# Kernel optimization log

Measured on AMD Instinct MI355X. Metric: run time of the kernel, lower is better.

## Reference

```python
import jax, jax.numpy as jnp
import numpy as np

N_NODES = 50000
N_EDGES = 800000


def setup_inputs() -> dict:
    key = jax.random.key(0)
    ks = jax.random.split(key, 10)
    x = jax.random.normal(ks[0], (N_NODES, 256), dtype=jnp.float32)
    edge_index = jax.random.randint(ks[1], (2, N_EDGES), 0, N_NODES, dtype=jnp.int64)
    edge_attr = jax.random.uniform(ks[2], (N_EDGES,), dtype=jnp.float32)
    def glorot(k, fan_in, fan_out):
        s = jnp.sqrt(6.0 / (fan_in + fan_out))
        return jax.random.uniform(k, (fan_in, fan_out), minval=-s, maxval=s, dtype=jnp.float32)
    W1 = glorot(ks[3], 256, 512); b1 = jnp.zeros((512,), jnp.float32)
    W2 = glorot(ks[4], 512, 256); b2 = jnp.zeros((256,), jnp.float32)
    W3 = glorot(ks[5], 256, 128); b3 = jnp.zeros((128,), jnp.float32)
    return {"x": x, "edge_index": edge_index, "edge_attr": edge_attr,
            "W1": W1, "b1": b1, "W2": W2, "b2": b2, "W3": W3, "b3": b3}


def _gcn_norm(edge_index, edge_attr, num_nodes):
    # PyG GCNConv default: add self-loops (weight 1), symmetric normalization.
    loops = jnp.arange(num_nodes, dtype=edge_index.dtype)
    src = jnp.concatenate([edge_index[0], loops])
    dst = jnp.concatenate([edge_index[1], loops])
    w = jnp.concatenate([edge_attr, jnp.ones((num_nodes,), edge_attr.dtype)])
    deg = jax.ops.segment_sum(w, dst, num_segments=num_nodes)
    dinv = jnp.where(deg > 0, jax.lax.rsqrt(deg), 0.0)
    norm = dinv[src] * w * dinv[dst]  # [E+N]
    return src, dst, norm


def _gcn_conv(h, W, b, src, dst, norm, num_nodes):
    h = h @ W                                   # [N, Dout] linear transform
    msg = h[src] * norm[:, None]                # gather + per-edge scale
    out = jax.ops.segment_sum(msg, dst, num_segments=num_nodes)  # scatter-add
    return out + b


def reference(x, edge_index, edge_attr, W1, b1, W2, b2, W3, b3):
    src, dst, norm = _gcn_norm(edge_index, edge_attr, N_NODES)
    h = jax.nn.relu(_gcn_conv(x, W1, b1, src, dst, norm, N_NODES))
    # dropout is identity in eval mode (reference runs with training=False)
    h = jax.nn.relu(_gcn_conv(h, W2, b2, src, dst, norm, N_NODES))
    h = _gcn_conv(h, W3, b3, src, dst, norm, N_NODES)
    return h.reshape(-1, h.shape[1])
```

## Files before the change

kernel.cpp:

```cpp
#include <hip/hip_runtime.h>
#include <cstdint>
#include <cstddef>

typedef unsigned short u16;
typedef unsigned int u32;

#define NN 50000
#define NE 800000

typedef __attribute__((ext_vector_type(8))) short bf16x8;
typedef __attribute__((ext_vector_type(4))) float f32x4;

__device__ __forceinline__ u16 f2bf(float f) {
  union { float f; u32 i; } v; v.f = f;
  return (u16)((v.i + 0x7FFFu + ((v.i >> 16) & 1u)) >> 16);
}
__device__ __forceinline__ void bf2x2(u32 w, float& a, float& b) {
  union { u32 i; float f; } lo, hi;
  lo.i = w << 16; hi.i = w & 0xFFFF0000u;
  a = lo.f; b = hi.f;
}
__device__ __forceinline__ void unpack8(const uint4& q, float* f) {
  bf2x2(q.x, f[0], f[1]); bf2x2(q.y, f[2], f[3]);
  bf2x2(q.z, f[4], f[5]); bf2x2(q.w, f[6], f[7]);
}

#define HIST_B 3125
#define XGROUPS (NN * 256 / 4)

__global__ void k_hist_cast(const int* __restrict__ dst,
                            int* __restrict__ cnt, int* __restrict__ slot,
                            const float* __restrict__ x, const float* __restrict__ W1,
                            const float* __restrict__ W2, const float* __restrict__ W3,
                            u16* __restrict__ xb, u16* __restrict__ Wt1,
                            u16* __restrict__ Wt2, u16* __restrict__ Wt3) {
  int b = blockIdx.x;
  if (b < HIST_B) {
    int e = b * 256 + threadIdx.x;
    if (e < NE) slot[e] = atomicAdd(&cnt[dst[e]], 1);
  } else {
    int i = (b - HIST_B) * 256 + threadIdx.x;
    if (i < XGROUPS) {
      float4 f = ((const float4*)x)[i];
      uint2 u;
      u.x = (u32)f2bf(f.x) | ((u32)f2bf(f.y) << 16);
      u.y = (u32)f2bf(f.z) | ((u32)f2bf(f.w) << 16);
      ((uint2*)xb)[i] = u;
    } else {
      int j = i - XGROUPS;
      if (j < 131072) {
        int k = j >> 9, n = j & 511;
        Wt1[n * 256 + k] = f2bf(W1[j]);
      } else if (j < 262144) {
        int j2 = j - 131072;
        int k = j2 >> 8, n = j2 & 255;
        Wt2[n * 512 + k] = f2bf(W2[j2]);
      } else if (j < 294912) {
        int j2 = j - 262144;
        int k = j2 >> 7, n = j2 & 127;
        Wt3[n * 256 + k] = f2bf(W3[j2]);
      }
    }
  }
}

__global__ void k_scan_part(const int* __restrict__ cnt, int* __restrict__ bsum, int n) {
  __shared__ int s[256];
  int i = blockIdx.x * 256 + threadIdx.x;
  s[threadIdx.x] = (i < n) ? cnt[i] : 0;
  __syncthreads();
  for (int o = 128; o > 0; o >>= 1) {
    if (threadIdx.x < o) s[threadIdx.x] += s[threadIdx.x + o];
    __syncthreads();
  }
  if (threadIdx.x == 0) bsum[blockIdx.x] = s[0];
}
__global__ void k_scan_fin(const int* __restrict__ cnt, const int* __restrict__ bsum,
                           int* __restrict__ rowptr, int n) {
  __shared__ int s[256];
  __shared__ int pre[256];
  int t = threadIdx.x;
  int i = blockIdx.x * 256 + t;
  pre[t] = (t < blockIdx.x) ? bsum[t] : 0;
  s[t] = (i < n) ? cnt[i] : 0;
  __syncthreads();
  for (int o = 128; o > 0; o >>= 1) {
    if (t < o) pre[t] += pre[t + o];
    __syncthreads();
  }
  if (t == 0) {
    int run = pre[0];
    for (int j = 0; j < 256; j++) { int v = s[j]; s[j] = run; run += v; }
  }
  __syncthreads();
  if (i < n) rowptr[i] = s[t];
}
__global__ void k_fill(const int* __restrict__ src, const int* __restrict__ dst,
                       const float* __restrict__ w, const int* __restrict__ rowptr,
                       const int* __restrict__ slot, uint2* __restrict__ edges, int E) {
  int e = blockIdx.x * 256 + threadIdx.x;
  if (e < E) {
    int d = dst[e];
    uint2 ev;
    ev.x = (u32)src[e];
    ev.y = __float_as_uint(w[e]);
    edges[rowptr[d] + slot[e]] = ev;
  }
}

__global__ __launch_bounds__(256) void k_sortrow(
    uint2* __restrict__ edges, const int* __restrict__ rowptr,
    const int* __restrict__ cnt, float* __restrict__ dinv, int n) {
  int wave = threadIdx.x >> 6, lane = threadIdx.x & 63;
  int row = blockIdx.x * 4 + wave;
  if (row >= n) return;
  int p = rowptr[row], c = cnt[row];
  if (c <= 64) {
    u32 kc = 0xFFFFFFFFu, kw = 0xFFFFFFFFu;
    if (lane < c) { uint2 e = edges[p + lane]; kc = e.x; kw = e.y; }
#pragma unroll
    for (int k = 2; k <= 64; k <<= 1) {
#pragma unroll
      for (int j = k >> 1; j > 0; j >>= 1) {
        u32 oc = __shfl_xor(kc, j, 64);
        u32 ow = __shfl_xor(kw, j, 64);
        bool up = ((lane & k) == 0);
        bool lower = ((lane & j) == 0);
        bool gt = (kc > oc) || (kc == oc && kw > ow);
        bool lt = (kc < oc) || (kc == oc && kw < ow);
        bool swap = up ? (lower ? gt : lt) : (lower ? lt : gt);
        if (swap) { kc = oc; kw = ow; }
      }
    }
    float s = (lane < c) ? __uint_as_float(kw) : 0.f;
#pragma unroll
    for (int off = 1; off < 64; off <<= 1) s += __shfl_xor(s, off, 64);
    if (lane < c) { uint2 e; e.x = kc; e.y = kw; edges[p + lane] = e; }
    if (lane == 0) dinv[row] = rsqrtf(1.0f + s);
  } else {
    if (lane == 0) {
      for (int i = 1; i < c; i++) {
        uint2 key = edges[p + i];
        int j2 = i - 1;
        while (j2 >= 0) {
          uint2 a = edges[p + j2];
          bool gt = (a.x > key.x) || (a.x == key.x && a.y > key.y);
          if (!gt) break;
          edges[p + j2 + 1] = a; j2--;
        }
        edges[p + j2 + 1] = key;
      }
      float s = 0.f;
      for (int i = 0; i < c; i++) s += __uint_as_float(edges[p + i].y);
      dinv[row] = rsqrtf(1.0f + s);
    }
  }
}

__global__ __launch_bounds__(256) void k_val(
    uint2* __restrict__ edges, const int* __restrict__ rowptr,
    const int* __restrict__ cnt, const float* __restrict__ dinv, int n) {
  int wave = threadIdx.x >> 6, lane = threadIdx.x & 63;
  int row = blockIdx.x * 4 + wave;
  if (row >= n) return;
  int p = rowptr[row], c = cnt[row];
  float dr = dinv[row];
  for (int l = lane; l < c; l += 64) {
    uint2 e = edges[p + l];
    float w = __uint_as_float(e.y);
    e.y = __float_as_uint(dinv[(int)e.x] * w * dr);
    edges[p + l] = e;
  }
}

template <int D, int OUTF32, int RELU, int HASB, int U>
__global__ __launch_bounds__(128) void k_agg(
    const u16* __restrict__ H, const int* __restrict__ rowptr,
    const int* __restrict__ cnt, const uint2* __restrict__ edges,
    const float* __restrict__ dinv,
    const float* __restrict__ bias, void* __restrict__ outv) {
  constexpr int RL = D / 8;
  constexpr int EPW = 64 / RL;
  int wave = threadIdx.x >> 6, lane = threadIdx.x & 63;
  int node = blockIdx.x * 2 + wave;
  if (node >= NN) return;
  const int sub = lane / RL;
  const int rl = lane & (RL - 1);
  const int base = rl * 8;
  float acc[8] = {};
  if (sub == 0) {
    float dv = dinv[node];
    float sw = dv * dv;
    uint4 q = *(const uint4*)(H + (size_t)node * D + base);
    float f[8]; unpack8(q, f);
#pragma unroll
    for (int j = 0; j < 8; j++) acc[j] = sw * f[j];
  }
  const int p = rowptr[node], c = cnt[node];
  for (int e0 = 0; e0 < c; e0 += EPW * U) {
    uint4 q[U];
    float v[U];
#pragma unroll
    for (int u = 0; u < U; u++) {
      int id = e0 + sub + u * EPW;
      bool ok = id < c;
      uint2 ev = edges[p + (ok ? id : 0)];
      v[u] = ok ? __uint_as_float(ev.y) : 0.f;
      int cs = ok ? (int)ev.x : node;
      q[u] = *(const uint4*)(H + (size_t)cs * D + base);
    }
#pragma unroll
    for (int u = 0; u < U; u++) {
      float f[8]; unpack8(q[u], f);
#pragma unroll
      for (int j = 0; j < 8; j++) acc[j] += v[u] * f[j];
    }
  }
#pragma unroll
  for (int j = 0; j < 8; j++) {
#pragma unroll
    for (int off = RL; off < 64; off <<= 1)
      acc[j] += __shfl_xor(acc[j], off, 64);
  }
  if (sub == 0) {
#pragma unroll
    for (int j = 0; j < 8; j++) {
      float v2 = acc[j];
      if (HASB) v2 += bias[base + j];
      if (RELU) v2 = fmaxf(v2, 0.f);
      acc[j] = v2;
    }
    if (OUTF32) {
      float* o = (float*)outv + (size_t)node * D + base;
      float4 f0 = {acc[0], acc[1], acc[2], acc[3]};
      float4 f1 = {acc[4], acc[5], acc[6], acc[7]};
      *(float4*)o = f0;
      *(float4*)(o + 4) = f1;
    } else {
      u16* o = (u16*)outv + (size_t)node * D + base;
      uint4 u;
      u.x = (u32)f2bf(acc[0]) | ((u32)f2bf(acc[1]) << 16);
      u.y = (u32)f2bf(acc[2]) | ((u32)f2bf(acc[3]) << 16);
      u.z = (u32)f2bf(acc[4]) | ((u32)f2bf(acc[5]) << 16);
      u.w = (u32)f2bf(acc[6]) | ((u32)f2bf(acc[7]) << 16);
      *(uint4*)o = u;
    }
  }
}

template <int RELU, int HASB, int NYB>
__global__ __launch_bounds__(512) void k_gemm(
    const u16* __restrict__ A, const u16* __restrict__ Bt,
    const float* __restrict__ bias, u16* __restrict__ C, int M, int Nd, int K) {
  __shared__ u16 As[256 * 64];
  __shared__ u16 Bs[128 * 64];
  const int tid = threadIdx.x;
  const int wave = tid >> 6, lane = tid & 63;
  const int nwg = gridDim.x;
  const int orig = blockIdx.x;
  const int xcd = orig & 7;
  const int q = nwg >> 3, r = nwg & 7;
  const int wgid = (xcd < r ? xcd * (q + 1) : r * (q + 1) + (xcd - r) * q) + (orig >> 3);
  const int m0 = (wgid / NYB) * 256, n0 = (wgid % NYB) * 128;
  const int wr = wave >> 1, wc = wave & 1;
  f32x4 acc[4][4] = {};

  for (int k0 = 0; k0 < K; k0 += 64) {
#pragma unroll
    for (int i = 0; i < 4; i++) {
      int rr = i * 64 + wave * 8 + (lane >> 3);
      int rg = m0 + rr; rg = rg < M ? rg : M - 1;
      const u16* ga = A + (size_t)rg * K + k0 + (lane & 7) * 8;
      __builtin_amdgcn_global_load_lds(
          (const __attribute__((address_space(1))) void*)ga,
          (__attribute__((address_space(3))) void*)&As[(i * 64 + wave * 8) * 64], 16, 0, 0);
    }
#pragma unroll
    for (int i = 0; i < 2; i++) {
      int rr = i * 64 + wave * 8 + (lane >> 3);
      int ng = n0 + rr;
      const u16* gb = Bt + (size_t)ng * K + k0 + (lane & 7) * 8;
      __builtin_amdgcn_global_load_lds(
          (const __attribute__((address_space(1))) void*)gb,
          (__attribute__((address_space(3))) void*)&Bs[(i * 64 + wave * 8) * 64], 16, 0, 0);
    }
    __syncthreads();
#pragma unroll
    for (int kk = 0; kk < 2; kk++) {
      bf16x8 af[4], bfr[4];
#pragma unroll
      for (int mi = 0; mi < 4; mi++)
        af[mi] = *(const bf16x8*)&As[(wr * 64 + mi * 16 + (lane & 15)) * 64 + kk * 32 + (lane >> 4) * 8];
#pragma unroll
      for (int ni = 0; ni < 4; ni++)
        bfr[ni] = *(const bf16x8*)&Bs[(wc * 64 + ni * 16 + (lane & 15)) * 64 + kk * 32 + (lane >> 4) * 8];
#pragma unroll
      for (int mi = 0; mi < 4; mi++)
#pragma unroll
        for (int ni = 0; ni < 4; ni++)
          acc[mi][ni] = __builtin_amdgcn_mfma_f32_16x16x32_bf16(af[mi], bfr[ni], acc[mi][ni], 0, 0, 0);
    }
    __syncthreads();
  }
  const int nb = n0 + wc * 64 + (lane & 15);
  float bv[4];
#pragma unroll
  for (int ni = 0; ni < 4; ni++) bv[ni] = HASB ? bias[nb + ni * 16] : 0.f;
#pragma unroll
  for (int mi = 0; mi < 4; mi++) {
#pragma unroll
    for (int rr = 0; rr < 4; rr++) {
      int row = m0 + wr * 64 + mi * 16 + (lane >> 4) * 4 + rr;
      if (row < M) {
#pragma unroll
        for (int ni = 0; ni < 4; ni++) {
          float v = acc[mi][ni][rr] + bv[ni];
          if (RELU) v = fmaxf(v, 0.f);
          C[(size_t)row * Nd + nb + ni * 16] = f2bf(v);
        }
      }
    }
  }
}

extern "C" void kernel_launch(void* const* d_in, const int* in_sizes, int n_in,
                              void* d_out, int out_size, void* d_ws, size_t ws_size,
                              hipStream_t stream) {
  const float* x  = (const float*)d_in[0];
  const int*   ei = (const int*)d_in[1];
  const float* ea = (const float*)d_in[2];
  const float* W1 = (const float*)d_in[3];
  const float* b1 = (const float*)d_in[4];
  const float* W2 = (const float*)d_in[5];
  const float* b2 = (const float*)d_in[6];
  const float* W3 = (const float*)d_in[7];
  const float* b3 = (const float*)d_in[8];
  const int* e_src = ei;
  const int* e_dst = ei + NE;

  size_t off = 0;
  auto carve = [&](size_t bytes) -> void* {
    void* r = (char*)d_ws + off;
    off += (bytes + 255) & ~(size_t)255;
    return r;
  };
  int*   counts = (int*)carve(NN * 4);
  float* dinv   = (float*)carve(NN * 4);
  int*   rowptr = (int*)carve(NN * 4);
  int*   bsum   = (int*)carve(256 * 4);
  int*   slot   = (int*)carve((size_t)NE * 4);
  uint2* edges  = (uint2*)carve((size_t)NE * 8);
  u16*   Wt1    = (u16*)carve(512 * 256 * 2);
  u16*   Wt2    = (u16*)carve(256 * 512 * 2);
  u16*   Wt3    = (u16*)carve(128 * 256 * 2);
  u16*   R0     = (u16*)carve((size_t)NN * 256 * 2);
  u16*   R1     = (u16*)carve((size_t)NN * 256 * 2);
  u16*   R2     = (u16*)carve((size_t)NN * 512 * 2);

  const int NB_N = (NN + 255) / 256;
  const int NB_E = (NE + 255) / 256;
  const int ROW_B = (NN + 3) / 4;
  const int AGG_B = (NN + 1) / 2;

  hipMemsetAsync(counts, 0, (size_t)NN * 4, stream);

  k_hist_cast<<<HIST_B + (XGROUPS + 294912 + 255) / 256, 256, 0, stream>>>(
      e_dst, counts, slot, x, W1, W2, W3, R0, Wt1, Wt2, Wt3);
  k_scan_part<<<NB_N, 256, 0, stream>>>(counts, bsum, NN);
  k_scan_fin<<<NB_N, 256, 0, stream>>>(counts, bsum, rowptr, NN);
  k_fill<<<NB_E, 256, 0, stream>>>(e_src, e_dst, ea, rowptr, slot, edges, NE);
  k_sortrow<<<ROW_B, 256, 0, stream>>>(edges, rowptr, counts, dinv, NN);
  k_val<<<ROW_B, 256, 0, stream>>>(edges, rowptr, counts, dinv, NN);

  k_agg<256, 0, 0, 0, 4><<<AGG_B, 128, 0, stream>>>(R0, rowptr, counts, edges, dinv, nullptr, R1);
  k_gemm<1, 1, 4><<<196 * 4, 512, 0, stream>>>(R1, Wt1, b1, R2, NN, 512, 256);
  k_gemm<0, 0, 2><<<196 * 2, 512, 0, stream>>>(R2, Wt2, nullptr, R0, NN, 256, 512);
  k_agg<256, 0, 1, 1, 4><<<AGG_B, 128, 0, stream>>>(R0, rowptr, counts, edges, dinv, b2, R1);
  k_gemm<0, 0, 1><<<196 * 1, 512, 0, stream>>>(R1, Wt3, nullptr, R0, NN, 128, 256);
  k_agg<128, 1, 0, 1, 4><<<AGG_B, 128, 0, stream>>>(R0, rowptr, counts, edges, dinv, b3, d_out);
}
```

Baseline: 345.8 us.

## Fuse edge-norm computation into first aggregation and interleave histogram with cast blocks

Removes the separate k_val kernel. The first aggregation pass now computes each edge's normalized weight from dinv, uses it, and writes it back into the edge list so the later passes can read it precomputed. The histogram/atomic blocks are also interleaved among the cast blocks, one in every 18 blocks, with each thread handling 4 edges, so that atomic traffic overlaps with streaming casts. The cost is an extra dinv gather plus an edge write inside the first aggregation, and extra index arithmetic in the block mapping.

```diff
diff --git a/kernel.cpp b/kernel.cpp
--- a/kernel.cpp
+++ b/kernel.cpp
@@ -25,8 +25,9 @@
   bf2x2(q.z, f[4], f[5]); bf2x2(q.w, f[6], f[7]);
 }
 
-#define HIST_B 3125
 #define XGROUPS (NN * 256 / 4)
+#define NA_B 782
+#define T_B 14455
 
 __global__ void k_hist_cast(const int* __restrict__ dst,
                             int* __restrict__ cnt, int* __restrict__ slot,
@@ -35,11 +36,27 @@
                             u16* __restrict__ xb, u16* __restrict__ Wt1,
                             u16* __restrict__ Wt2, u16* __restrict__ Wt3) {
   int b = blockIdx.x;
-  if (b < HIST_B) {
-    int e = b * 256 + threadIdx.x;
-    if (e < NE) slot[e] = atomicAdd(&cnt[dst[e]], 1);
+  int q = b / 18, r = b - q * 18;
+  if (r == 17) {
+    if (q >= NA_B) return;
+    int ebase = q * 1024 + threadIdx.x;
+    int ds[4]; bool ok[4];
+#pragma unroll
+    for (int u = 0; u < 4; u++) {
+      int e = ebase + u * 256;
+      ok[u] = e < NE;
+      ds[u] = ok[u] ? dst[e] : 0;
+    }
+    int sl[4];
+#pragma unroll
+    for (int u = 0; u < 4; u++)
+      if (ok[u]) sl[u] = atomicAdd(&cnt[ds[u]], 1);
+#pragma unroll
+    for (int u = 0; u < 4; u++)
+      if (ok[u]) slot[ebase + u * 256] = sl[u];
   } else {
-    int i = (b - HIST_B) * 256 + threadIdx.x;
+    int ci = b - q;
+    int i = ci * 256 + threadIdx.x;
     if (i < XGROUPS) {
       float4 f = ((const float4*)x)[i];
       uint2 u;
@@ -157,26 +174,10 @@
   }
 }
 
-__global__ __launch_bounds__(256) void k_val(
-    uint2* __restrict__ edges, const int* __restrict__ rowptr,
-    const int* __restrict__ cnt, const float* __restrict__ dinv, int n) {
-  int wave = threadIdx.x >> 6, lane = threadIdx.x & 63;
-  int row = blockIdx.x * 4 + wave;
-  if (row >= n) return;
-  int p = rowptr[row], c = cnt[row];
-  float dr = dinv[row];
-  for (int l = lane; l < c; l += 64) {
-    uint2 e = edges[p + l];
-    float w = __uint_as_float(e.y);
-    e.y = __float_as_uint(dinv[(int)e.x] * w * dr);
-    edges[p + l] = e;
-  }
-}
-
-template <int D, int OUTF32, int RELU, int HASB, int U>
+template <int D, int OUTF32, int RELU, int HASB, int U, int NORMIFY>
 __global__ __launch_bounds__(128) void k_agg(
     const u16* __restrict__ H, const int* __restrict__ rowptr,
-    const int* __restrict__ cnt, const uint2* __restrict__ edges,
+    const int* __restrict__ cnt, uint2* __restrict__ edges,
     const float* __restrict__ dinv,
     const float* __restrict__ bias, void* __restrict__ outv) {
   constexpr int RL = D / 8;
@@ -187,10 +188,10 @@
   const int sub = lane / RL;
   const int rl = lane & (RL - 1);
   const int base = rl * 8;
+  const float dvr = dinv[node];
   float acc[8] = {};
   if (sub == 0) {
-    float dv = dinv[node];
-    float sw = dv * dv;
+    float sw = dvr * dvr;
     uint4 q = *(const uint4*)(H + (size_t)node * D + base);
     float f[8]; unpack8(q, f);
 #pragma unroll
@@ -205,7 +206,16 @@
       int id = e0 + sub + u * EPW;
       bool ok = id < c;
       uint2 ev = edges[p + (ok ? id : 0)];
-      v[u] = ok ? __uint_as_float(ev.y) : 0.f;
+      float vv;
+      if (NORMIFY) {
+        int cs0 = (int)ev.x;
+        float wv = __uint_as_float(ev.y);
+        vv = dinv[cs0] * wv * dvr;
+        if (ok && rl == 0) edges[p + id].y = __float_as_uint(vv);
+      } else {
+        vv = __uint_as_float(ev.y);
+      }
+      v[u] = ok ? vv : 0.f;
       int cs = ok ? (int)ev.x : node;
       q[u] = *(const uint4*)(H + (size_t)cs * D + base);
     }
@@ -364,18 +374,17 @@
 
   hipMemsetAsync(counts, 0, (size_t)NN * 4, stream);
 
-  k_hist_cast<<<HIST_B + (XGROUPS + 294912 + 255) / 256, 256, 0, stream>>>(
+  k_hist_cast<<<T_B, 256, 0, stream>>>(
       e_dst, counts, slot, x, W1, W2, W3, R0, Wt1, Wt2, Wt3);
   k_scan_part<<<NB_N, 256, 0, stream>>>(counts, bsum, NN);
   k_scan_fin<<<NB_N, 256, 0, stream>>>(counts, bsum, rowptr, NN);
   k_fill<<<NB_E, 256, 0, stream>>>(e_src, e_dst, ea, rowptr, slot, edges, NE);
   k_sortrow<<<ROW_B, 256, 0, stream>>>(edges, rowptr, counts, dinv, NN);
-  k_val<<<ROW_B, 256, 0, stream>>>(edges, rowptr, counts, dinv, NN);
-
-  k_agg<256, 0, 0, 0, 4><<<AGG_B, 128, 0, stream>>>(R0, rowptr, counts, edges, dinv, nullptr, R1);
+
+  k_agg<256, 0, 0, 0, 4, 1><<<AGG_B, 128, 0, stream>>>(R0, rowptr, counts, edges, dinv, nullptr, R1);
   k_gemm<1, 1, 4><<<196 * 4, 512, 0, stream>>>(R1, Wt1, b1, R2, NN, 512, 256);
   k_gemm<0, 0, 2><<<196 * 2, 512, 0, stream>>>(R2, Wt2, nullptr, R0, NN, 256, 512);
-  k_agg<256, 0, 1, 1, 4><<<AGG_B, 128, 0, stream>>>(R0, rowptr, counts, edges, dinv, b2, R1);
+  k_agg<256, 0, 1, 1, 4, 0><<<AGG_B, 128, 0, stream>>>(R0, rowptr, counts, edges, dinv, b2, R1);
   k_gemm<0, 0, 1><<<196 * 1, 512, 0, stream>>>(R1, Wt3, nullptr, R0, NN, 128, 256);
-  k_agg<128, 1, 0, 1, 4><<<AGG_B, 128, 0, stream>>>(R0, rowptr, counts, edges, dinv, b3, d_out);
-}
+  k_agg<128, 1, 0, 1, 4, 0><<<AGG_B, 128, 0, stream>>>(R0, rowptr, counts, edges, dinv, b3, d_out);
+}
```

Measured after the change: 337.3 us. -2.5%, faster.
